# Kernel tuning notes

Measured on AMD Instinct MI355X. Metric: run time of the kernel, lower is better.

## Reference

```python
import jax, jax.numpy as jnp
import numpy as np

# dims: batch, dim_d, dim_k, in_ch, out_ch, length, kernel, pad, num segments
B, D, K, CI, CO, L, NB, P, S = 4, 32, 8, 2, 2, 4096, 15, 7, 8


def _segment_ids():
    # replicate PartiallyUnsharedConv1d.repeat_lengths logic
    padded = L + 2 * P
    rough = padded // S
    reps, tot = [], 0
    for i in range(S):
        r = (L - tot) if i == S - 1 else (rough - 2 * P)
        reps.append(r)
        tot += r
    return np.repeat(np.arange(S), reps)  # shape [L]


def setup_inputs() -> dict:
    key = jax.random.key(0)
    k1, k2, k3 = jax.random.split(key, 3)
    x = jax.random.normal(k1, (B, D, K, CI, L), dtype=jnp.float32)
    weight = 0.02 * jax.random.normal(k2, (D, K, CO, CI, S, 1, NB), dtype=jnp.float32)
    bias = 0.02 * jax.random.normal(k3, (D, K, CO, S, 1), dtype=jnp.float32)
    return {"x": x, "weight": weight, "bias": bias}


def reference(x, weight, bias):
    seg = jnp.asarray(_segment_ids())  # [L] segment id per output position
    # zero pad last dim (ConstantPad1d)
    xp = jnp.pad(x, ((0, 0), (0, 0), (0, 0), (0, 0), (P, P)))
    # unfold: sliding windows of size NB, stride 1 -> [b, d, k, i, L, NB]
    idx = jnp.arange(L)[:, None] + jnp.arange(NB)[None, :]
    xu = xp[..., idx]
    # gather per-position segment weights instead of python repeat/cat
    w = weight[:, :, :, :, seg, 0, :]  # [d, k, o, i, L, NB]
    out = jnp.einsum('dkoilf,bdkilf->bdkol', w, xu)  # [b, d, k, o, L]
    out = out + bias[:, :, :, seg, 0]  # bias broadcast over batch
    return out
```

## Files before the change

kernel.cpp:

```cpp
#include <hip/hip_runtime.h>
#include <stdint.h>

constexpr int Bc  = 4;
constexpr int Dc  = 32;
constexpr int Kc  = 8;
constexpr int CIc = 2;
constexpr int COc = 2;
constexpr int Lc  = 4096;
constexpr int NBc = 15;
constexpr int Sc  = 8;

constexpr int NTHREADS = 256;
constexpr int JT       = 4;
constexpr int TILE     = NTHREADS * JT;
constexpr int NTILES   = Lc / TILE;
constexpr int WELEMS   = COc * CIc * Sc * NBc;

typedef float f32x4 __attribute__((ext_vector_type(4)));
typedef const __attribute__((address_space(1))) float* gas1_t;
typedef __attribute__((address_space(3))) float* las3_t;

__device__ __forceinline__ int seg_of(int l) {
    int s = l / 499;
    return s > 7 ? 7 : s;
}

__global__ __launch_bounds__(NTHREADS) void cde_bcr_kernel(
    const float* __restrict__ x,
    const float* __restrict__ w,
    const float* __restrict__ bias,
    float* __restrict__ out)
{
    __shared__ __align__(16) float xs[CIc][Lc + 16];
    __shared__ __align__(16) float wl[COc * CIc * Sc][16];
    __shared__ float bl[COc * Sc];

    const int tid  = threadIdx.x;
    const int lane = tid & 63;
    const int wid  = tid >> 6;
    const int bdk  = blockIdx.x;
    const int dk   = bdk % (Dc * Kc);

    const float* xrow = x + (size_t)bdk * CIc * Lc;
#pragma unroll
    for (int i = 0; i < CIc; ++i) {
#pragma unroll
        for (int q = 0; q < 4; ++q) {
            const float* g = xrow + (size_t)i * Lc + q * 1024 + wid * 256 + lane * 4;
            float* lp = &xs[i][8 + q * 1024 + wid * 256];
            __builtin_amdgcn_global_load_lds((gas1_t)g, (las3_t)lp, 16, 0, 0);
        }
    }

    for (int t = tid; t < WELEMS; t += NTHREADS)
        wl[t / NBc][t % NBc] = w[(size_t)dk * WELEMS + t];
    if (tid < COc * Sc)
        bl[tid] = bias[(size_t)dk * (COc * Sc) + tid];

    if (tid < 2 * 16) {
        int i = tid >> 4, e = tid & 15;
        int idx = (e < 8) ? e : (Lc + e);
        xs[i][idx] = 0.0f;
    }

    __syncthreads();

    const float* wbase = &wl[0][0];

#pragma unroll
    for (int t = 0; t < NTILES; ++t) {
        const int gl0 = t * TILE + tid * JT;
        const int s0  = seg_of(gl0);
        const int s3  = seg_of(gl0 + JT - 1);

        float xa0[20], xa1[20];
#pragma unroll
        for (int m = 0; m < 5; ++m) {
            *(f32x4*)&xa0[4 * m] = *(const f32x4*)&xs[0][gl0 + 4 * m];
            *(f32x4*)&xa1[4 * m] = *(const f32x4*)&xs[1][gl0 + 4 * m];
        }

        float acc[COc][JT];
#pragma unroll
        for (int o = 0; o < COc; ++o)
#pragma unroll
            for (int j = 0; j < JT; ++j)
                acc[o][j] = bl[o * Sc + s0];

#pragma unroll
        for (int i = 0; i < CIc; ++i) {
            float wa[16], wb[16];
#pragma unroll
            for (int m = 0; m < 4; ++m) {
                *(f32x4*)&wa[4 * m] = *(const f32x4*)&wl[(0 * CIc + i) * Sc + s0][4 * m];
                *(f32x4*)&wb[4 * m] = *(const f32x4*)&wl[(1 * CIc + i) * Sc + s0][4 * m];
            }
#pragma unroll
            for (int f = 0; f < NBc; ++f) {
#pragma unroll
                for (int j = 0; j < JT; ++j) {
                    float xv = (i == 0) ? xa0[j + f + 1] : xa1[j + f + 1];
                    acc[0][j] = fmaf(wa[f], xv, acc[0][j]);
                    acc[1][j] = fmaf(wb[f], xv, acc[1][j]);
                }
            }
        }

        if (s3 != s0) {
            const int jstart = 499 * s3 - gl0;
            const float b0 = bl[0 * Sc + s3];
            const float b1 = bl[1 * Sc + s3];
#pragma unroll
            for (int j = 0; j < JT; ++j) {
                if (j >= jstart) {
                    float a0 = b0, a1 = b1;
#pragma unroll
                    for (int i = 0; i < CIc; ++i) {
#pragma unroll
                        for (int f = 0; f < NBc; ++f) {
                            float xv = (i == 0) ? xa0[j + f + 1] : xa1[j + f + 1];
                            a0 = fmaf(wl[(0 * CIc + i) * Sc + s3][f], xv, a0);
                            a1 = fmaf(wl[(1 * CIc + i) * Sc + s3][f], xv, a1);
                        }
                    }
                    acc[0][j] = a0;
                    acc[1][j] = a1;
                }
            }
        }

        float* ob = out + (size_t)bdk * COc * Lc + gl0;
        f32x4 v0 = { acc[0][0], acc[0][1], acc[0][2], acc[0][3] };
        f32x4 v1 = { acc[1][0], acc[1][1], acc[1][2], acc[1][3] };
        __builtin_nontemporal_store(v0, (f32x4*)(ob));
        __builtin_nontemporal_store(v1, (f32x4*)(ob + Lc));
    }
    (void)wbase;
}

extern "C" void kernel_launch(void* const* d_in, const int* in_sizes, int n_in,
                              void* d_out, int out_size, void* d_ws, size_t ws_size,
                              hipStream_t stream) {
    const float* x    = (const float*)d_in[0];
    const float* w    = (const float*)d_in[1];
    const float* bias = (const float*)d_in[2];
    float* out        = (float*)d_out;

    cde_bcr_kernel<<<dim3(Bc * Dc * Kc), NTHREADS, 0, stream>>>(x, w, bias, out);
}
```

Baseline: 18.77 us.

## Give each wave its own contiguous chunk and drop the block barrier

Each wavefront now stages and computes a contiguous 1024-element slice of the row. Every wave loads its own copy of the weights and bias into shared memory, and waits only on its own memory counters, so the block-wide __syncthreads goes away. Positions near chunk edges read their halo straight from global memory with zero-padding logic instead of relying on shared-memory padding. The trade-off is redundant weight and bias stores from all four waves to the same shared locations, plus extra divergent global loads for edge lanes.

```diff
diff --git a/kernel.cpp b/kernel.cpp
--- a/kernel.cpp
+++ b/kernel.cpp
@@ -12,8 +12,7 @@
 
 constexpr int NTHREADS = 256;
 constexpr int JT       = 4;
-constexpr int TILE     = NTHREADS * JT;
-constexpr int NTILES   = Lc / TILE;
+constexpr int CHUNK    = 1024;
 constexpr int WELEMS   = COc * CIc * Sc * NBc;
 
 typedef float f32x4 __attribute__((ext_vector_type(4)));
@@ -37,47 +36,52 @@
 
     const int tid  = threadIdx.x;
     const int lane = tid & 63;
-    const int wid  = tid >> 6;
+    const int wv   = tid >> 6;
     const int bdk  = blockIdx.x;
     const int dk   = bdk % (Dc * Kc);
 
     const float* xrow = x + (size_t)bdk * CIc * Lc;
+
 #pragma unroll
     for (int i = 0; i < CIc; ++i) {
 #pragma unroll
-        for (int q = 0; q < 4; ++q) {
-            const float* g = xrow + (size_t)i * Lc + q * 1024 + wid * 256 + lane * 4;
-            float* lp = &xs[i][8 + q * 1024 + wid * 256];
+        for (int q = 0; q < CHUNK / 256; ++q) {
+            const float* g = xrow + (size_t)i * Lc + wv * CHUNK + q * 256 + lane * 4;
+            float* lp = &xs[i][8 + wv * CHUNK + q * 256];
             __builtin_amdgcn_global_load_lds((gas1_t)g, (las3_t)lp, 16, 0, 0);
         }
     }
 
-    for (int t = tid; t < WELEMS; t += NTHREADS)
+    for (int t = lane; t < WELEMS; t += 64)
         wl[t / NBc][t % NBc] = w[(size_t)dk * WELEMS + t];
-    if (tid < COc * Sc)
-        bl[tid] = bias[(size_t)dk * (COc * Sc) + tid];
+    if (lane < COc * Sc)
+        bl[lane] = bias[(size_t)dk * (COc * Sc) + lane];
 
-    if (tid < 2 * 16) {
-        int i = tid >> 4, e = tid & 15;
-        int idx = (e < 8) ? e : (Lc + e);
-        xs[i][idx] = 0.0f;
-    }
-
-    __syncthreads();
-
-    const float* wbase = &wl[0][0];
+    asm volatile("s_waitcnt vmcnt(0) lgkmcnt(0)" ::: "memory");
+    __builtin_amdgcn_sched_barrier(0);
 
 #pragma unroll
-    for (int t = 0; t < NTILES; ++t) {
-        const int gl0 = t * TILE + tid * JT;
+    for (int t = 0; t < 4; ++t) {
+        const int low = t * 256 + lane * JT;
+        const int gl0 = wv * CHUNK + low;
         const int s0  = seg_of(gl0);
         const int s3  = seg_of(gl0 + JT - 1);
 
         float xa0[20], xa1[20];
+        if (low >= 8 && low <= CHUNK - 12) {
 #pragma unroll
-        for (int m = 0; m < 5; ++m) {
-            *(f32x4*)&xa0[4 * m] = *(const f32x4*)&xs[0][gl0 + 4 * m];
-            *(f32x4*)&xa1[4 * m] = *(const f32x4*)&xs[1][gl0 + 4 * m];
+            for (int m = 0; m < 5; ++m) {
+                *(f32x4*)&xa0[4 * m] = *(const f32x4*)&xs[0][gl0 + 4 * m];
+                *(f32x4*)&xa1[4 * m] = *(const f32x4*)&xs[1][gl0 + 4 * m];
+            }
+        } else {
+#pragma unroll
+            for (int m = 0; m < 20; ++m) {
+                int l = gl0 - 8 + m;
+                bool ok = (l >= 0 && l < Lc);
+                xa0[m] = ok ? xrow[l] : 0.0f;
+                xa1[m] = ok ? xrow[Lc + l] : 0.0f;
+            }
         }
 
         float acc[COc][JT];
@@ -135,7 +139,6 @@
         __builtin_nontemporal_store(v0, (f32x4*)(ob));
         __builtin_nontemporal_store(v1, (f32x4*)(ob + Lc));
     }
-    (void)wbase;
 }
 
 extern "C" void kernel_launch(void* const* d_in, const int* in_sizes, int n_in,
```

Result: slower. 20.94 us (+11.6%).

## Split each row into four L-quarter blocks with halo loads from global

Applied to the files above, without the earlier changes.

Each block now handles one 1024-wide quarter of a (b,d,k) row instead of the whole row, giving four times as many blocks with a quarter of the shared memory each. Edge threads whose windows cross the quarter boundary read their halo directly from global memory with bounds checks instead of from shared memory. The intent is more parallelism and occupancy on a 1024-block grid. The cost is that weights and bias are reloaded four times per row, and the boundary threads take a slower, divergent path.

```diff
diff --git a/kernel.cpp b/kernel.cpp
--- a/kernel.cpp
+++ b/kernel.cpp
@@ -13,7 +13,7 @@
 constexpr int NTHREADS = 256;
 constexpr int JT       = 4;
 constexpr int TILE     = NTHREADS * JT;
-constexpr int NTILES   = Lc / TILE;
+constexpr int NQ       = Lc / TILE;
 constexpr int WELEMS   = COc * CIc * Sc * NBc;
 
 typedef float f32x4 __attribute__((ext_vector_type(4)));
@@ -31,25 +31,23 @@
     const float* __restrict__ bias,
     float* __restrict__ out)
 {
-    __shared__ __align__(16) float xs[CIc][Lc + 16];
+    __shared__ __align__(16) float xs[CIc][TILE + 16];
     __shared__ __align__(16) float wl[COc * CIc * Sc][16];
     __shared__ float bl[COc * Sc];
 
-    const int tid  = threadIdx.x;
-    const int lane = tid & 63;
-    const int wid  = tid >> 6;
-    const int bdk  = blockIdx.x;
-    const int dk   = bdk % (Dc * Kc);
+    const int tid   = threadIdx.x;
+    const int lane  = tid & 63;
+    const int wv    = tid >> 6;
+    const int row   = blockIdx.x >> 2;
+    const int qbase = (blockIdx.x & 3) * TILE;
+    const int dk    = row % (Dc * Kc);
 
-    const float* xrow = x + (size_t)bdk * CIc * Lc;
+    const float* xrow = x + (size_t)row * CIc * Lc;
 #pragma unroll
     for (int i = 0; i < CIc; ++i) {
-#pragma unroll
-        for (int q = 0; q < 4; ++q) {
-            const float* g = xrow + (size_t)i * Lc + q * 1024 + wid * 256 + lane * 4;
-            float* lp = &xs[i][8 + q * 1024 + wid * 256];
-            __builtin_amdgcn_global_load_lds((gas1_t)g, (las3_t)lp, 16, 0, 0);
-        }
+        const float* g = xrow + (size_t)i * Lc + qbase + wv * 256 + lane * 4;
+        __builtin_amdgcn_global_load_lds((gas1_t)g,
+            (las3_t)&xs[i][8 + wv * 256], 16, 0, 0);
     }
 
     for (int t = tid; t < WELEMS; t += NTHREADS)
@@ -57,85 +55,84 @@
     if (tid < COc * Sc)
         bl[tid] = bias[(size_t)dk * (COc * Sc) + tid];
 
-    if (tid < 2 * 16) {
-        int i = tid >> 4, e = tid & 15;
-        int idx = (e < 8) ? e : (Lc + e);
-        xs[i][idx] = 0.0f;
+    __syncthreads();
+
+    const int low = tid * JT;
+    const int gl0 = qbase + low;
+    const int s0  = seg_of(gl0);
+    const int s3  = seg_of(gl0 + JT - 1);
+
+    float xa0[20], xa1[20];
+    if (low >= 8 && low <= TILE - 12) {
+#pragma unroll
+        for (int m = 0; m < 5; ++m) {
+            *(f32x4*)&xa0[4 * m] = *(const f32x4*)&xs[0][low + 4 * m];
+            *(f32x4*)&xa1[4 * m] = *(const f32x4*)&xs[1][low + 4 * m];
+        }
+    } else {
+#pragma unroll
+        for (int m = 0; m < 20; ++m) {
+            int l = gl0 - 8 + m;
+            bool ok = (l >= 0 && l < Lc);
+            xa0[m] = ok ? xrow[l] : 0.0f;
+            xa1[m] = ok ? xrow[Lc + l] : 0.0f;
+        }
     }
 
-    __syncthreads();
-
-    const float* wbase = &wl[0][0];
+    float acc[COc][JT];
+#pragma unroll
+    for (int o = 0; o < COc; ++o)
+#pragma unroll
+        for (int j = 0; j < JT; ++j)
+            acc[o][j] = bl[o * Sc + s0];
 
 #pragma unroll
-    for (int t = 0; t < NTILES; ++t) {
-        const int gl0 = t * TILE + tid * JT;
-        const int s0  = seg_of(gl0);
-        const int s3  = seg_of(gl0 + JT - 1);
-
-        float xa0[20], xa1[20];
+    for (int i = 0; i < CIc; ++i) {
+        float wa[16], wb[16];
 #pragma unroll
-        for (int m = 0; m < 5; ++m) {
-            *(f32x4*)&xa0[4 * m] = *(const f32x4*)&xs[0][gl0 + 4 * m];
-            *(f32x4*)&xa1[4 * m] = *(const f32x4*)&xs[1][gl0 + 4 * m];
+        for (int m = 0; m < 4; ++m) {
+            *(f32x4*)&wa[4 * m] = *(const f32x4*)&wl[(0 * CIc + i) * Sc + s0][4 * m];
+            *(f32x4*)&wb[4 * m] = *(const f32x4*)&wl[(1 * CIc + i) * Sc + s0][4 * m];
         }
-
-        float acc[COc][JT];
 #pragma unroll
-        for (int o = 0; o < COc; ++o)
+        for (int f = 0; f < NBc; ++f) {
 #pragma unroll
-            for (int j = 0; j < JT; ++j)
-                acc[o][j] = bl[o * Sc + s0];
-
-#pragma unroll
-        for (int i = 0; i < CIc; ++i) {
-            float wa[16], wb[16];
-#pragma unroll
-            for (int m = 0; m < 4; ++m) {
-                *(f32x4*)&wa[4 * m] = *(const f32x4*)&wl[(0 * CIc + i) * Sc + s0][4 * m];
-                *(f32x4*)&wb[4 * m] = *(const f32x4*)&wl[(1 * CIc + i) * Sc + s0][4 * m];
-            }
-#pragma unroll
-            for (int f = 0; f < NBc; ++f) {
-#pragma unroll
-                for (int j = 0; j < JT; ++j) {
-                    float xv = (i == 0) ? xa0[j + f + 1] : xa1[j + f + 1];
-                    acc[0][j] = fmaf(wa[f], xv, acc[0][j]);
-                    acc[1][j] = fmaf(wb[f], xv, acc[1][j]);
-                }
+            for (int j = 0; j < JT; ++j) {
+                float xv = (i == 0) ? xa0[j + f + 1] : xa1[j + f + 1];
+                acc[0][j] = fmaf(wa[f], xv, acc[0][j]);
+                acc[1][j] = fmaf(wb[f], xv, acc[1][j]);
             }
         }
+    }
 
-        if (s3 != s0) {
-            const int jstart = 499 * s3 - gl0;
-            const float b0 = bl[0 * Sc + s3];
-            const float b1 = bl[1 * Sc + s3];
+    if (s3 != s0) {
+        const int jstart = 499 * s3 - gl0;
+        const float b0 = bl[0 * Sc + s3];
+        const float b1 = bl[1 * Sc + s3];
 #pragma unroll
-            for (int j = 0; j < JT; ++j) {
-                if (j >= jstart) {
-                    float a0 = b0, a1 = b1;
+        for (int j = 0; j < JT; ++j) {
+            if (j >= jstart) {
+                float a0 = b0, a1 = b1;
 #pragma unroll
-                    for (int i = 0; i < CIc; ++i) {
+                for (int i = 0; i < CIc; ++i) {
 #pragma unroll
-                        for (int f = 0; f < NBc; ++f) {
-                            float xv = (i == 0) ? xa0[j + f + 1] : xa1[j + f + 1];
-                            a0 = fmaf(wl[(0 * CIc + i) * Sc + s3][f], xv, a0);
-                            a1 = fmaf(wl[(1 * CIc + i) * Sc + s3][f], xv, a1);
-                        }
+                    for (int f = 0; f < NBc; ++f) {
+                        float xv = (i == 0) ? xa0[j + f + 1] : xa1[j + f + 1];
+                        a0 = fmaf(wl[(0 * CIc + i) * Sc + s3][f], xv, a0);
+                        a1 = fmaf(wl[(1 * CIc + i) * Sc + s3][f], xv, a1);
                     }
-                    acc[0][j] = a0;
-                    acc[1][j] = a1;
                 }
+                acc[0][j] = a0;
+                acc[1][j] = a1;
             }
         }
+    }
 
-        float* ob = out + (size_t)bdk * COc * Lc + gl0;
-        f32x4 v0 = { acc[0][0], acc[0][1], acc[0][2], acc[0][3] };
-        f32x4 v1 = { acc[1][0], acc[1][1], acc[1][2], acc[1][3] };
-        __builtin_nontemporal_store(v0, (f32x4*)(ob));
-        __builtin_nontemporal_store(v1, (f32x4*)(ob + Lc));
-    }
-    (void)wbase;
+    float* ob = out + (size_t)row * COc * Lc + gl0;
+    f32x4 v0 = { acc[0][0], acc[0][1], acc[0][2], acc[0][3] };
+    f32x4 v1 = { acc[1][0], acc[1][1], acc[1][2], acc[1][3] };
+    __builtin_nontemporal_store(v0, (f32x4*)(ob));
+    __builtin_nontemporal_store(v1, (f32x4*)(ob + Lc));
 }
 
 extern "C" void kernel_launch(void* const* d_in, const int* in_sizes, int n_in,
@@ -146,5 +143,5 @@
     const float* bias = (const float*)d_in[2];
     float* out        = (float*)d_out;
 
-    cde_bcr_kernel<<<dim3(Bc * Dc * Kc), NTHREADS, 0, stream>>>(x, w, bias, out);
+    cde_bcr_kernel<<<dim3(Bc * Dc * Kc * NQ), NTHREADS, 0, stream>>>(x, w, bias, out);
 }
```

After: 22.40 us. 1.19x slower.
